# Kernel tuning notes

Measured on AMD Instinct MI355X. Metric: run time of the kernel, lower is better.

Reference implementation:

```python
import jax, jax.numpy as jnp
import numpy as np

H, W, C = 64, 64, 2048
IMG = 224


def setup_inputs() -> dict:
    key = jax.random.key(0)
    features = jax.random.normal(key, (2, H, W, C), dtype=jnp.float32)
    return {"features": features, "img_size": IMG}


def reference(features, img_size):
    # features: [2, H, W, C] -- query (index 0) and target (index 1) feature maps.
    x0 = features[0]  # [H, W, C]
    x1 = features[1]  # [H, W, C]
    # Correlation volume: Decomposition[i,j,k,l] = sum_c x0[i,j,c] * x1[k,l,c]
    # (replaces the quadruple Python loop with a single GEMM-shaped einsum)
    decom = jnp.einsum('ijc,klc->ijkl', x0, x1)  # [H, W, H, W]
    decom = decom / jnp.max(decom)
    # NOTE: source calls `Decomposition.clamp(min=0)` without assignment -> no-op.
    decom_1 = jnp.sum(decom, axis=(2, 3))  # [H, W] saliency on query image
    decom_2 = jnp.sum(decom, axis=(0, 1))  # [H, W] saliency on target image
    stacked = jnp.stack((decom_1, decom_2))  # [2, H, W]
    # F.interpolate(mode='bilinear', align_corners=False) == half-pixel bilinear resize
    out = jax.image.resize(stacked, (2, img_size, img_size), method='bilinear')
    return out  # [2, img_size, img_size]
```

## Files before the change

### kernel.cpp

```cpp
#include <hip/hip_runtime.h>
#include <hip/hip_bf16.h>

#define HW    4096
#define CDIM  2048
#define IMG   224
#define NTKI  64
#define NTM   128
#define LROW  528
#define QSCALE 21.166666f
#define NS    32

typedef int   int4v  __attribute__((ext_vector_type(4)));
typedef int   i32x16 __attribute__((ext_vector_type(16)));
typedef char  char4v __attribute__((ext_vector_type(4)));

__device__ __forceinline__ i32x16 zi16() {
    i32x16 z;
#pragma unroll
    for (int i = 0; i < 16; ++i) z[i] = 0;
    return z;
}
__device__ __forceinline__ char quant8(float x) {
    int r = __float2int_rn(x * QSCALE);
    r = min(max(r, -127), 127);
    return (char)r;
}

__device__ __forceinline__ void gload_lds16(const char* g, char* l) {
    __builtin_amdgcn_global_load_lds(
        (const __attribute__((address_space(1))) void*)g,
        (__attribute__((address_space(3))) void*)l, 16, 0, 0);
}

__global__ __launch_bounds__(256) void convert_pack_partial(
    const float* __restrict__ feat,
    char* __restrict__ Ap, char* __restrict__ Bp,
    float* __restrict__ P) {
    __shared__ char lds[64 * LROW];
    __shared__ float csum[512];
    const int tid = threadIdx.x;
    const int mat = blockIdx.z;
    const int rm  = blockIdx.y;
    const int kb0 = blockIdx.x * 512;
    const float* src = feat + (size_t)mat * HW * CDIM + (size_t)(rm * 64) * CDIM + kb0;

    const int cc = (tid & 127) * 4;
    float a0 = 0.f, a1 = 0.f, a2 = 0.f, a3 = 0.f;
#pragma unroll
    for (int j = 0; j < 32; ++j) {
        const int r = j * 2 + (tid >> 7);
        float4 v = *(const float4*)&src[(size_t)r * CDIM + cc];
        a0 += v.x; a1 += v.y; a2 += v.z; a3 += v.w;
        char4v q;
        q[0] = quant8(v.x); q[1] = quant8(v.y);
        q[2] = quant8(v.z); q[3] = quant8(v.w);
        *(char4v*)&lds[r * LROW + cc] = q;
    }
    if (tid >= 128) {
        csum[cc + 0] = a0; csum[cc + 1] = a1;
        csum[cc + 2] = a2; csum[cc + 3] = a3;
    }
    __syncthreads();
    if (tid < 128) {
        float4 p;
        p.x = a0 + csum[cc + 0]; p.y = a1 + csum[cc + 1];
        p.z = a2 + csum[cc + 2]; p.w = a3 + csum[cc + 3];
        *(float4*)&P[((size_t)mat * 64 + rm) * CDIM + kb0 + cc] = p;
    }

    const int l = tid & 63, w = tid >> 6;
    char* dstbase = mat ? Bp : Ap;
#pragma unroll
    for (int i = 0; i < 8; ++i) {
        const int t = w * 8 + i;
        const int tml = t >> 4, tkl = t & 15;
        int4v v = *(const int4v*)
            &lds[(tml * 32 + (l & 31)) * LROW + tkl * 32 + (l >> 5) * 16];
        const int tm  = rm * 2 + tml;
        const int tkg = blockIdx.x * 16 + tkl;
        *(int4v*)&dstbase[((size_t)(tm * NTKI + tkg) * 64 + l) * 16] = v;
    }
}

__global__ __launch_bounds__(512, 2) void gemm_max_kernel(
    const char* __restrict__ Ap, const char* __restrict__ Bp,
    const float* __restrict__ P, float* __restrict__ s,
    float* __restrict__ blockmax) {
    __shared__ char lds[4 * 32768];
    __shared__ int wred[8];
    const int tid  = threadIdx.x;
    const int lane = tid & 63;
    const int wave = tid >> 6;
    const int wm = wave >> 2, wn = wave & 3;
    const int bm = blockIdx.y, bn = blockIdx.x;

    const char* gb[4];
    int loff[4];
#pragma unroll
    for (int q = 0; q < 4; ++q) {
        const int c = wave * 4 + q;
        const int kk = c & 1;
        if (c < 16) {
            const int il = c >> 1;
            gb[q] = Ap + ((size_t)(bm * 8 + il) * NTKI + kk) * 1024 + lane * 16;
            loff[q] = (il * 2 + kk) * 1024;
        } else {
            const int jl = (c - 16) >> 1;
            gb[q] = Bp + ((size_t)(bn * 8 + jl) * NTKI + kk) * 1024 + lane * 16;
            loff[q] = 16384 + (jl * 2 + kk) * 1024;
        }
    }

#define ISSUE_STAGE(S) do {                                         \
        char* buf_ = lds + (((S) & 3) << 15);                       \
        _Pragma("unroll")                                           \
        for (int q = 0; q < 4; ++q)                                 \
            gload_lds16(gb[q] + (size_t)(S) * 2048, buf_ + loff[q]);\
    } while (0)

    ISSUE_STAGE(0); ISSUE_STAGE(1); ISSUE_STAGE(2);

    if (bm == 0 && bn < 16 && tid < 256) {
        const int gc = bn * 256 + tid;
        const float* Pp = P + (size_t)(gc >> 11) * 64 * CDIM + (gc & 2047);
        float sum = 0.f;
#pragma unroll 8
        for (int r = 0; r < 64; ++r) sum += Pp[(size_t)r * CDIM];
        s[gc] = sum;
    }

    asm volatile("s_waitcnt vmcnt(8)" ::: "memory");
    asm volatile("s_barrier" ::: "memory");

    const int abase = wm * 8192 + lane * 16;
    const int bbase = 16384 + wn * 4096 + lane * 16;

    i32x16 acc00 = zi16(), acc01 = zi16();
    i32x16 acc10 = zi16(), acc11 = zi16();
    i32x16 acc20 = zi16(), acc21 = zi16();
    i32x16 acc30 = zi16(), acc31 = zi16();

    for (int st = 0; st < NS; ++st) {
        if (st + 3 < NS) ISSUE_STAGE(st + 3);

        const char* base = lds + ((st & 3) << 15);
#pragma unroll
        for (int kk = 0; kk < 2; ++kk) {
            const char* ab = base + abase + kk * 1024;
            const char* bb = base + bbase + kk * 1024;
            int4v a0 = *(const int4v*)(ab);
            int4v a1 = *(const int4v*)(ab + 2048);
            int4v a2 = *(const int4v*)(ab + 4096);
            int4v a3 = *(const int4v*)(ab + 6144);
            int4v b0 = *(const int4v*)(bb);
            int4v b1 = *(const int4v*)(bb + 2048);
            __builtin_amdgcn_s_setprio(1);
            acc00 = __builtin_amdgcn_mfma_i32_32x32x32_i8(a0, b0, acc00, 0, 0, 0);
            acc01 = __builtin_amdgcn_mfma_i32_32x32x32_i8(a0, b1, acc01, 0, 0, 0);
            acc10 = __builtin_amdgcn_mfma_i32_32x32x32_i8(a1, b0, acc10, 0, 0, 0);
            acc11 = __builtin_amdgcn_mfma_i32_32x32x32_i8(a1, b1, acc11, 0, 0, 0);
            acc20 = __builtin_amdgcn_mfma_i32_32x32x32_i8(a2, b0, acc20, 0, 0, 0);
            acc21 = __builtin_amdgcn_mfma_i32_32x32x32_i8(a2, b1, acc21, 0, 0, 0);
            acc30 = __builtin_amdgcn_mfma_i32_32x32x32_i8(a3, b0, acc30, 0, 0, 0);
            acc31 = __builtin_amdgcn_mfma_i32_32x32x32_i8(a3, b1, acc31, 0, 0, 0);
            __builtin_amdgcn_s_setprio(0);
        }

        if (st < NS - 3)      { asm volatile("s_waitcnt vmcnt(8)" ::: "memory"); }
        else if (st == NS - 3){ asm volatile("s_waitcnt vmcnt(4)" ::: "memory"); }
        else if (st == NS - 2){ asm volatile("s_waitcnt vmcnt(0)" ::: "memory"); }
        if (st < NS - 1) asm volatile("s_barrier" ::: "memory");
    }
#undef ISSUE_STAGE

    int m = INT_MIN;
#pragma unroll
    for (int i = 0; i < 16; ++i) {
        m = max(m, acc00[i]); m = max(m, acc01[i]);
        m = max(m, acc10[i]); m = max(m, acc11[i]);
        m = max(m, acc20[i]); m = max(m, acc21[i]);
        m = max(m, acc30[i]); m = max(m, acc31[i]);
    }
#pragma unroll
    for (int off = 32; off; off >>= 1)
        m = max(m, __shfl_down(m, off));
    if (lane == 0) wred[wave] = m;
    __syncthreads();
    if (tid == 0) {
        int im = wred[0];
#pragma unroll
        for (int w2 = 1; w2 < 8; ++w2) im = max(im, wred[w2]);
        blockmax[blockIdx.y * gridDim.x + blockIdx.x] =
            (float)im * (1.0f / (QSCALE * QSCALE));
    }
}

__global__ __launch_bounds__(256) void saliency_kernel(
    const float* __restrict__ feat, const float* __restrict__ s,
    float* __restrict__ sal) {
    const int tid = threadIdx.x, lane = tid & 63, wave = tid >> 6;
    const int g = blockIdx.x * 4 + wave;
    const float* x;
    const float* sv;
    if (g < HW) { x = feat + (size_t)g * CDIM;                            sv = s + CDIM; }
    else        { x = feat + (size_t)HW * CDIM + (size_t)(g - HW) * CDIM; sv = s; }
    float acc = 0.f;
#pragma unroll
    for (int it = 0; it < 8; ++it) {
        const int c0 = it * 256 + lane * 4;
        float4 v = *(const float4*)&x[c0];
        float4 w = *(const float4*)&sv[c0];
        acc += v.x * w.x + v.y * w.y + v.z * w.z + v.w * w.w;
    }
#pragma unroll
    for (int off = 32; off; off >>= 1) acc += __shfl_down(acc, off);
    if (lane == 0) sal[g] = acc;
}

__global__ __launch_bounds__(256) void resize_kernel(
    const float* __restrict__ sal, const float* __restrict__ bmax,
    float* __restrict__ out) {
    __shared__ float w[4];
    __shared__ float rM;
    const int tid = threadIdx.x;
    float m = -3.4e38f;
    for (int i = tid; i < 256; i += 256) m = fmaxf(m, bmax[i]);
#pragma unroll
    for (int off = 32; off; off >>= 1) m = fmaxf(m, __shfl_down(m, off));
    if ((tid & 63) == 0) w[tid >> 6] = m;
    __syncthreads();
    if (tid == 0)
        rM = 1.0f / fmaxf(fmaxf(w[0], w[1]), fmaxf(w[2], w[3]));
    __syncthreads();

    const int idx = blockIdx.x * 256 + tid;
    if (idx >= 2 * IMG * IMG) return;
    const int ch = idx / (IMG * IMG);
    const int rem = idx % (IMG * IMG);
    const int oy = rem / IMG, ox = rem % IMG;
    const float scale = 64.0f / (float)IMG;
    const float sy = ((float)oy + 0.5f) * scale - 0.5f;
    const float sx = ((float)ox + 0.5f) * scale - 0.5f;
    const float fy0 = floorf(sy), fx0 = floorf(sx);
    const float wy = sy - fy0, wx = sx - fx0;
    int y0 = (int)fy0, x0 = (int)fx0;
    int y1 = min(max(y0 + 1, 0), 63), x1 = min(max(x0 + 1, 0), 63);
    y0 = min(max(y0, 0), 63); x0 = min(max(x0, 0), 63);
    const float* p = sal + ch * HW;
    const float v00 = p[y0 * 64 + x0], v01 = p[y0 * 64 + x1];
    const float v10 = p[y1 * 64 + x0], v11 = p[y1 * 64 + x1];
    out[idx] = ((1.f - wy) * ((1.f - wx) * v00 + wx * v01) +
                wy * ((1.f - wx) * v10 + wx * v11)) * rM;
}

extern "C" void kernel_launch(void* const* d_in, const int* in_sizes, int n_in,
                              void* d_out, int out_size, void* d_ws, size_t ws_size,
                              hipStream_t stream) {
    const float* feat = (const float*)d_in[0];
    float* out = (float*)d_out;

    char* ws = (char*)d_ws;
    char* Ap = ws;
    char* Bp = ws + (size_t)8 * 1024 * 1024;
    float* P    = (float*)(ws + (size_t)16 * 1024 * 1024);
    float* s    = P + 2 * 64 * CDIM;
    float* bmax = s + 2 * CDIM;
    float* sal  = bmax + 1024;

    convert_pack_partial<<<dim3(4, 64, 2), 256, 0, stream>>>(feat, Ap, Bp, P);
    gemm_max_kernel<<<dim3(16, 16), 512, 0, stream>>>(Ap, Bp, P, s, bmax);
    saliency_kernel<<<2048, 256, 0, stream>>>(feat, s, sal);
    const int nout = 2 * IMG * IMG;
    resize_kernel<<<(nout + 255) / 256, 256, 0, stream>>>(sal, bmax, out);
}
```

Before: 144.9 us.

## Use 4 waves with 128x128 warp tiles and software-pipelined LDS fragment loads

Cuts the GEMM block from 8 waves to 4. Each wave now computes a 128x128 sub-tile with 16 accumulators instead of 8, which raises MFMA reuse per LDS fragment load. The k-loop is restructured so the next stage's fragments are prefetched from LDS while the current MFMAs run, and the wait and barrier move to the top of the loop. In exchange, fewer waves are available to hide latency, and the larger accumulator set raises register pressure, with launch bounds set to one block.

Measured after the change: 261.5 us. 1.8x slower.

```diff
diff --git a/kernel.cpp b/kernel.cpp
--- a/kernel.cpp
+++ b/kernel.cpp
@@ -82,23 +82,23 @@
     }
 }
 
-__global__ __launch_bounds__(512, 2) void gemm_max_kernel(
+__global__ __launch_bounds__(256, 1) void gemm_max_kernel(
     const char* __restrict__ Ap, const char* __restrict__ Bp,
     const float* __restrict__ P, float* __restrict__ s,
     float* __restrict__ blockmax) {
     __shared__ char lds[4 * 32768];
-    __shared__ int wred[8];
+    __shared__ int wred[4];
     const int tid  = threadIdx.x;
     const int lane = tid & 63;
     const int wave = tid >> 6;
-    const int wm = wave >> 2, wn = wave & 3;
+    const int wm = wave >> 1, wn = wave & 1;
     const int bm = blockIdx.y, bn = blockIdx.x;
 
-    const char* gb[4];
-    int loff[4];
-#pragma unroll
-    for (int q = 0; q < 4; ++q) {
-        const int c = wave * 4 + q;
+    const char* gb[8];
+    int loff[8];
+#pragma unroll
+    for (int q = 0; q < 8; ++q) {
+        const int c = wave * 8 + q;
         const int kk = c & 1;
         if (c < 16) {
             const int il = c >> 1;
@@ -114,13 +114,13 @@
 #define ISSUE_STAGE(S) do {                                         \
         char* buf_ = lds + (((S) & 3) << 15);                       \
         _Pragma("unroll")                                           \
-        for (int q = 0; q < 4; ++q)                                 \
+        for (int q = 0; q < 8; ++q)                                 \
             gload_lds16(gb[q] + (size_t)(S) * 2048, buf_ + loff[q]);\
     } while (0)
 
     ISSUE_STAGE(0); ISSUE_STAGE(1); ISSUE_STAGE(2);
 
-    if (bm == 0 && bn < 16 && tid < 256) {
+    if (bm == 0 && bn < 16) {
         const int gc = bn * 256 + tid;
         const float* Pp = P + (size_t)(gc >> 11) * 64 * CDIM + (gc & 2047);
         float sum = 0.f;
@@ -129,57 +129,80 @@
         s[gc] = sum;
     }
 
-    asm volatile("s_waitcnt vmcnt(8)" ::: "memory");
+    asm volatile("s_waitcnt vmcnt(16)" ::: "memory");
     asm volatile("s_barrier" ::: "memory");
 
-    const int abase = wm * 8192 + lane * 16;
-    const int bbase = 16384 + wn * 4096 + lane * 16;
-
-    i32x16 acc00 = zi16(), acc01 = zi16();
-    i32x16 acc10 = zi16(), acc11 = zi16();
-    i32x16 acc20 = zi16(), acc21 = zi16();
-    i32x16 acc30 = zi16(), acc31 = zi16();
+    const int aoff = wm * 8192 + lane * 16;
+    const int boff = 16384 + wn * 8192 + lane * 16;
+
+    i32x16 c00 = zi16(), c01 = zi16(), c02 = zi16(), c03 = zi16();
+    i32x16 c10 = zi16(), c11 = zi16(), c12 = zi16(), c13 = zi16();
+    i32x16 c20 = zi16(), c21 = zi16(), c22 = zi16(), c23 = zi16();
+    i32x16 c30 = zi16(), c31 = zi16(), c32 = zi16(), c33 = zi16();
+
+#define MM(i, j, A, B) c##i##j = __builtin_amdgcn_mfma_i32_32x32x32_i8(A, B, c##i##j, 0, 0, 0)
+#define MFMA16(A0,A1,A2,A3,B0,B1,B2,B3) do {                \
+        __builtin_amdgcn_s_setprio(1);                      \
+        MM(0,0,A0,B0); MM(0,1,A0,B1); MM(0,2,A0,B2); MM(0,3,A0,B3); \
+        MM(1,0,A1,B0); MM(1,1,A1,B1); MM(1,2,A1,B2); MM(1,3,A1,B3); \
+        MM(2,0,A2,B0); MM(2,1,A2,B1); MM(2,2,A2,B2); MM(2,3,A2,B3); \
+        MM(3,0,A3,B0); MM(3,1,A3,B1); MM(3,2,A3,B2); MM(3,3,A3,B3); \
+        __builtin_amdgcn_s_setprio(0);                      \
+    } while (0)
+
+    const char* b0p = lds + aoff;
+    const char* b0q = lds + boff;
+    int4v a0 = *(const int4v*)(b0p);
+    int4v a1 = *(const int4v*)(b0p + 2048);
+    int4v a2 = *(const int4v*)(b0p + 4096);
+    int4v a3 = *(const int4v*)(b0p + 6144);
+    int4v b0 = *(const int4v*)(b0q);
+    int4v b1 = *(const int4v*)(b0q + 2048);
+    int4v b2 = *(const int4v*)(b0q + 4096);
+    int4v b3 = *(const int4v*)(b0q + 6144);
 
     for (int st = 0; st < NS; ++st) {
+        if (st < NS - 2) { asm volatile("s_waitcnt vmcnt(8)" ::: "memory"); }
+        else             { asm volatile("s_waitcnt vmcnt(0)" ::: "memory"); }
+        asm volatile("s_barrier" ::: "memory");
         if (st + 3 < NS) ISSUE_STAGE(st + 3);
 
-        const char* base = lds + ((st & 3) << 15);
-#pragma unroll
-        for (int kk = 0; kk < 2; ++kk) {
-            const char* ab = base + abase + kk * 1024;
-            const char* bb = base + bbase + kk * 1024;
-            int4v a0 = *(const int4v*)(ab);
-            int4v a1 = *(const int4v*)(ab + 2048);
-            int4v a2 = *(const int4v*)(ab + 4096);
-            int4v a3 = *(const int4v*)(ab + 6144);
-            int4v b0 = *(const int4v*)(bb);
-            int4v b1 = *(const int4v*)(bb + 2048);
-            __builtin_amdgcn_s_setprio(1);
-            acc00 = __builtin_amdgcn_mfma_i32_32x32x32_i8(a0, b0, acc00, 0, 0, 0);
-            acc01 = __builtin_amdgcn_mfma_i32_32x32x32_i8(a0, b1, acc01, 0, 0, 0);
-            acc10 = __builtin_amdgcn_mfma_i32_32x32x32_i8(a1, b0, acc10, 0, 0, 0);
-            acc11 = __builtin_amdgcn_mfma_i32_32x32x32_i8(a1, b1, acc11, 0, 0, 0);
-            acc20 = __builtin_amdgcn_mfma_i32_32x32x32_i8(a2, b0, acc20, 0, 0, 0);
-            acc21 = __builtin_amdgcn_mfma_i32_32x32x32_i8(a2, b1, acc21, 0, 0, 0);
-            acc30 = __builtin_amdgcn_mfma_i32_32x32x32_i8(a3, b0, acc30, 0, 0, 0);
-            acc31 = __builtin_amdgcn_mfma_i32_32x32x32_i8(a3, b1, acc31, 0, 0, 0);
-            __builtin_amdgcn_s_setprio(0);
-        }
-
-        if (st < NS - 3)      { asm volatile("s_waitcnt vmcnt(8)" ::: "memory"); }
-        else if (st == NS - 3){ asm volatile("s_waitcnt vmcnt(4)" ::: "memory"); }
-        else if (st == NS - 2){ asm volatile("s_waitcnt vmcnt(0)" ::: "memory"); }
-        if (st < NS - 1) asm volatile("s_barrier" ::: "memory");
+        const char* ab = lds + ((st & 3) << 15) + aoff;
+        const char* bb = lds + ((st & 3) << 15) + boff;
+        const char* nab = lds + (((st + 1) & 3) << 15) + aoff;
+        const char* nbb = lds + (((st + 1) & 3) << 15) + boff;
+
+        int4v xa0 = *(const int4v*)(ab + 1024);
+        int4v xa1 = *(const int4v*)(ab + 2048 + 1024);
+        int4v xa2 = *(const int4v*)(ab + 4096 + 1024);
+        int4v xa3 = *(const int4v*)(ab + 6144 + 1024);
+        int4v xb0 = *(const int4v*)(bb + 1024);
+        int4v xb1 = *(const int4v*)(bb + 2048 + 1024);
+        int4v xb2 = *(const int4v*)(bb + 4096 + 1024);
+        int4v xb3 = *(const int4v*)(bb + 6144 + 1024);
+        MFMA16(a0, a1, a2, a3, b0, b1, b2, b3);
+
+        a0 = *(const int4v*)(nab);
+        a1 = *(const int4v*)(nab + 2048);
+        a2 = *(const int4v*)(nab + 4096);
+        a3 = *(const int4v*)(nab + 6144);
+        b0 = *(const int4v*)(nbb);
+        b1 = *(const int4v*)(nbb + 2048);
+        b2 = *(const int4v*)(nbb + 4096);
+        b3 = *(const int4v*)(nbb + 6144);
+        MFMA16(xa0, xa1, xa2, xa3, xb0, xb1, xb2, xb3);
     }
 #undef ISSUE_STAGE
+#undef MFMA16
+#undef MM
 
     int m = INT_MIN;
 #pragma unroll
     for (int i = 0; i < 16; ++i) {
-        m = max(m, acc00[i]); m = max(m, acc01[i]);
-        m = max(m, acc10[i]); m = max(m, acc11[i]);
-        m = max(m, acc20[i]); m = max(m, acc21[i]);
-        m = max(m, acc30[i]); m = max(m, acc31[i]);
+        m = max(m, c00[i]); m = max(m, c01[i]); m = max(m, c02[i]); m = max(m, c03[i]);
+        m = max(m, c10[i]); m = max(m, c11[i]); m = max(m, c12[i]); m = max(m, c13[i]);
+        m = max(m, c20[i]); m = max(m, c21[i]); m = max(m, c22[i]); m = max(m, c23[i]);
+        m = max(m, c30[i]); m = max(m, c31[i]); m = max(m, c32[i]); m = max(m, c33[i]);
     }
 #pragma unroll
     for (int off = 32; off; off >>= 1)
@@ -187,9 +210,7 @@
     if (lane == 0) wred[wave] = m;
     __syncthreads();
     if (tid == 0) {
-        int im = wred[0];
-#pragma unroll
-        for (int w2 = 1; w2 < 8; ++w2) im = max(im, wred[w2]);
+        const int im = max(max(wred[0], wred[1]), max(wred[2], wred[3]));
         blockmax[blockIdx.y * gridDim.x + blockIdx.x] =
             (float)im * (1.0f / (QSCALE * QSCALE));
     }
@@ -268,7 +289,7 @@
     float* sal  = bmax + 1024;
 
     convert_pack_partial<<<dim3(4, 64, 2), 256, 0, stream>>>(feat, Ap, Bp, P);
-    gemm_max_kernel<<<dim3(16, 16), 512, 0, stream>>>(Ap, Bp, P, s, bmax);
+    gemm_max_kernel<<<dim3(16, 16), 256, 0, stream>>>(Ap, Bp, P, s, bmax);
     saliency_kernel<<<2048, 256, 0, stream>>>(feat, s, sal);
     const int nout = 2 * IMG * IMG;
     resize_kernel<<<(nout + 255) / 256, 256, 0, stream>>>(sal, bmax, out);
```

## Software-pipeline LDS fragment loads against MFMA in int8 GEMM main loop

Applied to the files above, without the earlier changes.

Restructures the K-stage loop so the LDS fragment reads for the second k-half are issued before the first half's MFMAs run. The next stage's first-half fragments are prefetched into registers before the second half's MFMAs. The global-load wait and barrier move to mid-iteration, and the next ISSUE_STAGE follows the barrier. The aim is to hide LDS read latency behind matrix instructions, in exchange for more live vector registers and a changed wait schedule. The final iteration also does a harmless extra read from an unused buffer.

Result: no change. 144.4 us (-0.4%).

```diff
diff --git a/kernel.cpp b/kernel.cpp
--- a/kernel.cpp
+++ b/kernel.cpp
@@ -132,46 +132,62 @@
     asm volatile("s_waitcnt vmcnt(8)" ::: "memory");
     asm volatile("s_barrier" ::: "memory");
 
-    const int abase = wm * 8192 + lane * 16;
-    const int bbase = 16384 + wn * 4096 + lane * 16;
+    const int aoff = wm * 8192 + lane * 16;
+    const int boff = 16384 + wn * 4096 + lane * 16;
 
     i32x16 acc00 = zi16(), acc01 = zi16();
     i32x16 acc10 = zi16(), acc11 = zi16();
     i32x16 acc20 = zi16(), acc21 = zi16();
     i32x16 acc30 = zi16(), acc31 = zi16();
 
+#define MM(i, j, A, B) acc##i##j = __builtin_amdgcn_mfma_i32_32x32x32_i8(A, B, acc##i##j, 0, 0, 0)
+#define MFMA8(A0,A1,A2,A3,B0,B1) do {               \
+        __builtin_amdgcn_s_setprio(1);              \
+        MM(0,0,A0,B0); MM(0,1,A0,B1);               \
+        MM(1,0,A1,B0); MM(1,1,A1,B1);               \
+        MM(2,0,A2,B0); MM(2,1,A2,B1);               \
+        MM(3,0,A3,B0); MM(3,1,A3,B1);               \
+        __builtin_amdgcn_s_setprio(0);              \
+    } while (0)
+
+    int4v a0 = *(const int4v*)(lds + aoff);
+    int4v a1 = *(const int4v*)(lds + aoff + 2048);
+    int4v a2 = *(const int4v*)(lds + aoff + 4096);
+    int4v a3 = *(const int4v*)(lds + aoff + 6144);
+    int4v b0 = *(const int4v*)(lds + boff);
+    int4v b1 = *(const int4v*)(lds + boff + 2048);
+
     for (int st = 0; st < NS; ++st) {
+        const char* ab  = lds + ((st & 3) << 15) + aoff;
+        const char* bb  = lds + ((st & 3) << 15) + boff;
+        const char* nab = lds + (((st + 1) & 3) << 15) + aoff;
+        const char* nbb = lds + (((st + 1) & 3) << 15) + boff;
+
+        int4v xa0 = *(const int4v*)(ab + 1024);
+        int4v xa1 = *(const int4v*)(ab + 2048 + 1024);
+        int4v xa2 = *(const int4v*)(ab + 4096 + 1024);
+        int4v xa3 = *(const int4v*)(ab + 6144 + 1024);
+        int4v xb0 = *(const int4v*)(bb + 1024);
+        int4v xb1 = *(const int4v*)(bb + 2048 + 1024);
+        MFMA8(a0, a1, a2, a3, b0, b1);
+
+        if (st < NS - 2) { asm volatile("s_waitcnt vmcnt(4)" ::: "memory"); }
+        else             { asm volatile("s_waitcnt vmcnt(0)" ::: "memory"); }
+        asm volatile("s_barrier" ::: "memory");
+
         if (st + 3 < NS) ISSUE_STAGE(st + 3);
 
-        const char* base = lds + ((st & 3) << 15);
-#pragma unroll
-        for (int kk = 0; kk < 2; ++kk) {
-            const char* ab = base + abase + kk * 1024;
-            const char* bb = base + bbase + kk * 1024;
-            int4v a0 = *(const int4v*)(ab);
-            int4v a1 = *(const int4v*)(ab + 2048);
-            int4v a2 = *(const int4v*)(ab + 4096);
-            int4v a3 = *(const int4v*)(ab + 6144);
-            int4v b0 = *(const int4v*)(bb);
-            int4v b1 = *(const int4v*)(bb + 2048);
-            __builtin_amdgcn_s_setprio(1);
-            acc00 = __builtin_amdgcn_mfma_i32_32x32x32_i8(a0, b0, acc00, 0, 0, 0);
-            acc01 = __builtin_amdgcn_mfma_i32_32x32x32_i8(a0, b1, acc01, 0, 0, 0);
-            acc10 = __builtin_amdgcn_mfma_i32_32x32x32_i8(a1, b0, acc10, 0, 0, 0);
-            acc11 = __builtin_amdgcn_mfma_i32_32x32x32_i8(a1, b1, acc11, 0, 0, 0);
-            acc20 = __builtin_amdgcn_mfma_i32_32x32x32_i8(a2, b0, acc20, 0, 0, 0);
-            acc21 = __builtin_amdgcn_mfma_i32_32x32x32_i8(a2, b1, acc21, 0, 0, 0);
-            acc30 = __builtin_amdgcn_mfma_i32_32x32x32_i8(a3, b0, acc30, 0, 0, 0);
-            acc31 = __builtin_amdgcn_mfma_i32_32x32x32_i8(a3, b1, acc31, 0, 0, 0);
-            __builtin_amdgcn_s_setprio(0);
-        }
-
-        if (st < NS - 3)      { asm volatile("s_waitcnt vmcnt(8)" ::: "memory"); }
-        else if (st == NS - 3){ asm volatile("s_waitcnt vmcnt(4)" ::: "memory"); }
-        else if (st == NS - 2){ asm volatile("s_waitcnt vmcnt(0)" ::: "memory"); }
-        if (st < NS - 1) asm volatile("s_barrier" ::: "memory");
+        a0 = *(const int4v*)(nab);
+        a1 = *(const int4v*)(nab + 2048);
+        a2 = *(const int4v*)(nab + 4096);
+        a3 = *(const int4v*)(nab + 6144);
+        b0 = *(const int4v*)(nbb);
+        b1 = *(const int4v*)(nbb + 2048);
+        MFMA8(xa0, xa1, xa2, xa3, xb0, xb1);
     }
 #undef ISSUE_STAGE
+#undef MFMA8
+#undef MM
 
     int m = INT_MIN;
 #pragma unroll
```

## Halve GEMM N-tile, triple-buffer LDS, double grid for higher occupancy

Applied to the files above, without the earlier changes.

Shrinks the int8 GEMM block tile from 256x256 to 256x128, giving each wave a 64x64 output with four accumulators. The LDS pipeline drops from four stages to three, launch bounds allow four blocks per CU, and the grid doubles to 512 blocks, with the resize kernel now reducing 512 block maxima. LDS reads are hoisted ahead of the next stage's issue. The aim is better CU fill and occupancy on a 256-CU part, at the cost of lower arithmetic intensity per block and more redundant A-tile loads.

New measurement: 140.5 us. 1.03x faster.

```diff
diff --git a/kernel.cpp b/kernel.cpp
--- a/kernel.cpp
+++ b/kernel.cpp
@@ -9,6 +9,7 @@
 #define LROW  528
 #define QSCALE 21.166666f
 #define NS    32
+#define SBUF  24576
 
 typedef int   int4v  __attribute__((ext_vector_type(4)));
 typedef int   i32x16 __attribute__((ext_vector_type(16)));
@@ -82,45 +83,45 @@
     }
 }
 
-__global__ __launch_bounds__(512, 2) void gemm_max_kernel(
+__global__ __launch_bounds__(512, 4) void gemm_max_kernel(
     const char* __restrict__ Ap, const char* __restrict__ Bp,
     const float* __restrict__ P, float* __restrict__ s,
     float* __restrict__ blockmax) {
-    __shared__ char lds[4 * 32768];
+    __shared__ char lds[3 * SBUF];
     __shared__ int wred[8];
     const int tid  = threadIdx.x;
     const int lane = tid & 63;
     const int wave = tid >> 6;
-    const int wm = wave >> 2, wn = wave & 3;
+    const int wm = wave >> 1, wn = wave & 1;
     const int bm = blockIdx.y, bn = blockIdx.x;
 
-    const char* gb[4];
-    int loff[4];
-#pragma unroll
-    for (int q = 0; q < 4; ++q) {
-        const int c = wave * 4 + q;
+    const char* gb[3];
+    int loff[3];
+#pragma unroll
+    for (int q = 0; q < 3; ++q) {
+        const int c = wave * 3 + q;
         const int kk = c & 1;
         if (c < 16) {
             const int il = c >> 1;
             gb[q] = Ap + ((size_t)(bm * 8 + il) * NTKI + kk) * 1024 + lane * 16;
-            loff[q] = (il * 2 + kk) * 1024;
+            loff[q] = il * 2048 + kk * 1024;
         } else {
             const int jl = (c - 16) >> 1;
-            gb[q] = Bp + ((size_t)(bn * 8 + jl) * NTKI + kk) * 1024 + lane * 16;
-            loff[q] = 16384 + (jl * 2 + kk) * 1024;
+            gb[q] = Bp + ((size_t)(bn * 4 + jl) * NTKI + kk) * 1024 + lane * 16;
+            loff[q] = 16384 + jl * 2048 + kk * 1024;
         }
     }
 
 #define ISSUE_STAGE(S) do {                                         \
-        char* buf_ = lds + (((S) & 3) << 15);                       \
+        char* buf_ = lds + ((S) % 3) * SBUF;                        \
         _Pragma("unroll")                                           \
-        for (int q = 0; q < 4; ++q)                                 \
+        for (int q = 0; q < 3; ++q)                                 \
             gload_lds16(gb[q] + (size_t)(S) * 2048, buf_ + loff[q]);\
     } while (0)
 
-    ISSUE_STAGE(0); ISSUE_STAGE(1); ISSUE_STAGE(2);
-
-    if (bm == 0 && bn < 16 && tid < 256) {
+    ISSUE_STAGE(0); ISSUE_STAGE(1);
+
+    if (bm == 15 && bn < 16 && tid < 256) {
         const int gc = bn * 256 + tid;
         const float* Pp = P + (size_t)(gc >> 11) * 64 * CDIM + (gc & 2047);
         float sum = 0.f;
@@ -129,57 +130,52 @@
         s[gc] = sum;
     }
 
-    asm volatile("s_waitcnt vmcnt(8)" ::: "memory");
+    asm volatile("s_waitcnt vmcnt(3)" ::: "memory");
     asm volatile("s_barrier" ::: "memory");
 
-    const int abase = wm * 8192 + lane * 16;
-    const int bbase = 16384 + wn * 4096 + lane * 16;
+    const int aoff = wm * 2 * 2048 + lane * 16;
+    const int boff = 16384 + wn * 2 * 2048 + lane * 16;
 
     i32x16 acc00 = zi16(), acc01 = zi16();
     i32x16 acc10 = zi16(), acc11 = zi16();
-    i32x16 acc20 = zi16(), acc21 = zi16();
-    i32x16 acc30 = zi16(), acc31 = zi16();
+
+#define MM(i, j, A, B) acc##i##j = __builtin_amdgcn_mfma_i32_32x32x32_i8(A, B, acc##i##j, 0, 0, 0)
 
     for (int st = 0; st < NS; ++st) {
-        if (st + 3 < NS) ISSUE_STAGE(st + 3);
-
-        const char* base = lds + ((st & 3) << 15);
-#pragma unroll
-        for (int kk = 0; kk < 2; ++kk) {
-            const char* ab = base + abase + kk * 1024;
-            const char* bb = base + bbase + kk * 1024;
-            int4v a0 = *(const int4v*)(ab);
-            int4v a1 = *(const int4v*)(ab + 2048);
-            int4v a2 = *(const int4v*)(ab + 4096);
-            int4v a3 = *(const int4v*)(ab + 6144);
-            int4v b0 = *(const int4v*)(bb);
-            int4v b1 = *(const int4v*)(bb + 2048);
-            __builtin_amdgcn_s_setprio(1);
-            acc00 = __builtin_amdgcn_mfma_i32_32x32x32_i8(a0, b0, acc00, 0, 0, 0);
-            acc01 = __builtin_amdgcn_mfma_i32_32x32x32_i8(a0, b1, acc01, 0, 0, 0);
-            acc10 = __builtin_amdgcn_mfma_i32_32x32x32_i8(a1, b0, acc10, 0, 0, 0);
-            acc11 = __builtin_amdgcn_mfma_i32_32x32x32_i8(a1, b1, acc11, 0, 0, 0);
-            acc20 = __builtin_amdgcn_mfma_i32_32x32x32_i8(a2, b0, acc20, 0, 0, 0);
-            acc21 = __builtin_amdgcn_mfma_i32_32x32x32_i8(a2, b1, acc21, 0, 0, 0);
-            acc30 = __builtin_amdgcn_mfma_i32_32x32x32_i8(a3, b0, acc30, 0, 0, 0);
-            acc31 = __builtin_amdgcn_mfma_i32_32x32x32_i8(a3, b1, acc31, 0, 0, 0);
-            __builtin_amdgcn_s_setprio(0);
-        }
-
-        if (st < NS - 3)      { asm volatile("s_waitcnt vmcnt(8)" ::: "memory"); }
-        else if (st == NS - 3){ asm volatile("s_waitcnt vmcnt(4)" ::: "memory"); }
-        else if (st == NS - 2){ asm volatile("s_waitcnt vmcnt(0)" ::: "memory"); }
-        if (st < NS - 1) asm volatile("s_barrier" ::: "memory");
+        const char* base = lds + (st % 3) * SBUF;
+        const char* ab = base + aoff;
+        const char* bb = base + boff;
+
+        int4v a0k0 = *(const int4v*)(ab);
+        int4v a1k0 = *(const int4v*)(ab + 2048);
+        int4v a0k1 = *(const int4v*)(ab + 1024);
+        int4v a1k1 = *(const int4v*)(ab + 2048 + 1024);
+        int4v b0k0 = *(const int4v*)(bb);
+        int4v b1k0 = *(const int4v*)(bb + 2048);
+        int4v b0k1 = *(const int4v*)(bb + 1024);
+        int4v b1k1 = *(const int4v*)(bb + 2048 + 1024);
+
+        if (st + 2 < NS) ISSUE_STAGE(st + 2);
+
+        __builtin_amdgcn_s_setprio(1);
+        MM(0,0, a0k0, b0k0); MM(0,1, a0k0, b1k0);
+        MM(1,0, a1k0, b0k0); MM(1,1, a1k0, b1k0);
+        MM(0,0, a0k1, b0k1); MM(0,1, a0k1, b1k1);
+        MM(1,0, a1k1, b0k1); MM(1,1, a1k1, b1k1);
+        __builtin_amdgcn_s_setprio(0);
+
+        if (st < NS - 2) { asm volatile("s_waitcnt vmcnt(3)" ::: "memory"); }
+        else             { asm volatile("s_waitcnt vmcnt(0)" ::: "memory"); }
+        if (st < NS - 1) { asm volatile("s_barrier" ::: "memory"); }
     }
 #undef ISSUE_STAGE
+#undef MM
 
     int m = INT_MIN;
 #pragma unroll
     for (int i = 0; i < 16; ++i) {
         m = max(m, acc00[i]); m = max(m, acc01[i]);
         m = max(m, acc10[i]); m = max(m, acc11[i]);
-        m = max(m, acc20[i]); m = max(m, acc21[i]);
-        m = max(m, acc30[i]); m = max(m, acc31[i]);
     }
 #pragma unroll
     for (int off = 32; off; off >>= 1)
@@ -224,7 +220,7 @@
     __shared__ float rM;
     const int tid = threadIdx.x;
     float m = -3.4e38f;
-    for (int i = tid; i < 256; i += 256) m = fmaxf(m, bmax[i]);
+    for (int i = tid; i < 512; i += 256) m = fmaxf(m, bmax[i]);
 #pragma unroll
     for (int off = 32; off; off >>= 1) m = fmaxf(m, __shfl_down(m, off));
     if ((tid & 63) == 0) w[tid >> 6] = m;
@@ -268,7 +264,7 @@
     float* sal  = bmax + 1024;
 
     convert_pack_partial<<<dim3(4, 64, 2), 256, 0, stream>>>(feat, Ap, Bp, P);
-    gemm_max_kernel<<<dim3(16, 16), 512, 0, stream>>>(Ap, Bp, P, s, bmax);
+    gemm_max_kernel<<<dim3(32, 16), 512, 0, stream>>>(Ap, Bp, P, s, bmax);
     saliency_kernel<<<2048, 256, 0, stream>>>(feat, s, sal);
     const int nout = 2 * IMG * IMG;
     resize_kernel<<<(nout + 255) / 256, 256, 0, stream>>>(sal, bmax, out);
```
